# Kernel optimization log

Hardware: AMD Instinct MI355X
Metric: run time of the kernel (lower is better)

The kernel has to match this reference:

```python
import jax, jax.numpy as jnp
import numpy as np

B, L, D = 4, 4096, 1024
DS, EXP, DC = 16, 2, 4
DI = EXP * D
K_SYM = max(3, 2 * DC + 1)  # 9


def _linear(x, w, b):
    # torch nn.Linear: y = x @ W^T + b, W:[out,in]
    return jnp.einsum('blc,oc->blo', x, w) + b


def _dwconv(x, kernel, bias, pad_l, pad_r):
    # x:[B,L,C], kernel:[C,1,k] depthwise, torch 'same' padding (asymmetric for even k)
    y = jax.lax.conv_general_dilated(
        x.transpose(0, 2, 1), kernel, window_strides=(1,),
        padding=[(pad_l, pad_r)], dimension_numbers=('NCH', 'OIH', 'NCH'),
        feature_group_count=x.shape[-1])
    return y.transpose(0, 2, 1) + bias


def _rmsnorm(x, w, eps=1e-6):
    scale = jax.lax.rsqrt(jnp.mean(x * x, axis=-1, keepdims=True) + eps)
    return w * x * scale


def setup_inputs() -> dict:
    key = jax.random.key(0)
    ks = jax.random.split(key, 12)
    def n(k, shape, s=0.02):
        return jax.random.normal(k, shape, jnp.float32) * s
    return {
        'x': jax.random.normal(ks[0], (B, L, D), jnp.float32),
        'norm_w': jnp.ones((D,), jnp.float32),
        'in_w': n(ks[1], (2 * DI, D)), 'in_b': jnp.zeros((2 * DI,), jnp.float32),
        'dwa_k': n(ks[2], (DI, 1, DC)), 'dwa_b': jnp.zeros((DI,), jnp.float32),
        'A': n(ks[3], (DI, DS)), 'Bm': n(ks[4], (DS, DI)),
        'sym_k': n(ks[5], (DI, 1, K_SYM)), 'sym_b': jnp.zeros((DI,), jnp.float32),
        'pw_w': n(ks[6], (DI, DI)), 'pw_b': jnp.zeros((DI,), jnp.float32),
        'ha_w': n(ks[7], (DI // 2, DI)), 'ha_b': jnp.zeros((DI // 2,), jnp.float32),
        'hb_w': n(ks[8], (DI // 2, DI)), 'hb_b': jnp.zeros((DI // 2,), jnp.float32),
        'fuse_w': n(ks[9], (DI, DI)), 'fuse_b': jnp.zeros((DI,), jnp.float32),
        'out_w': n(ks[10], (D, DI)), 'out_b': jnp.zeros((D,), jnp.float32),
    }


def reference(x, norm_w, in_w, in_b, dwa_k, dwa_b, A, Bm, sym_k, sym_b,
              pw_w, pw_b, ha_w, ha_b, hb_w, hb_b, fuse_w, fuse_b, out_w, out_b):
    residual = x
    h = _rmsnorm(x, norm_w)
    h = _linear(h, in_w, in_b)                       # [B,L,2*DI]
    gate, val = h[..., :DI], h[..., DI:]
    gate = jax.nn.sigmoid(gate)
    # mamba-like branch: depthwise conv (k=4, torch 'same' -> pad (1,2)) + low-rank A@B
    a = _dwconv(val, dwa_k, dwa_b, 1, 2)             # [B,L,DI]
    a = jnp.einsum('bld,ds->bls', a, A)              # [B,L,DS]
    a = jnp.einsum('bls,sd->bld', a, Bm)             # [B,L,DI]
    # symmetric conv branch: depthwise conv (k=9, pad (4,4)) -> silu -> pointwise linear
    b = _dwconv(val, sym_k, sym_b, K_SYM // 2, K_SYM // 2)
    b = jax.nn.silu(b)
    b = _linear(b, pw_w, pw_b)
    a = _linear(a, ha_w, ha_b)                       # [B,L,DI/2]
    b = _linear(b, hb_w, hb_b)                       # [B,L,DI/2]
    y = jnp.concatenate([a, b], axis=-1)             # [B,L,DI]
    y = _linear(y, fuse_w, fuse_b)
    y = gate * y
    y = _linear(y, out_w, out_b)                     # [B,L,D]
    return residual + y
```

## Files before the change

kernel.cpp:

```cpp
#include <hip/hip_runtime.h>
#include <hip/hip_bf16.h>
#include <stdint.h>

typedef __bf16 bf16;
typedef __bf16 bf16x8 __attribute__((ext_vector_type(8)));
typedef __bf16 bf16x4 __attribute__((ext_vector_type(4)));
typedef float  f32x4  __attribute__((ext_vector_type(4)));

#define LDS_PTR(p) ((__attribute__((address_space(3))) uint32_t*)(p))
#define GLB_PTR(p) ((const __attribute__((address_space(1))) uint32_t*)(p))

static constexpr int BATCH = 4, SEQ = 4096, DMODEL = 1024;
static constexpr int DI = 2048;
static constexpr int MTOK = BATCH * SEQ;

enum { EPI_SPLIT = 0, EPI_PLAIN = 1, EPI_GATEADD = 2, EPI_RES = 3, EPI_F32S = 4 };

template <int EPI, bool SPLITK = false>
__global__ __launch_bounds__(256) void gemm_bt(
    const bf16* __restrict__ Aact, const bf16* __restrict__ W,
    const float* __restrict__ bias,
    bf16* __restrict__ out0, bf16* __restrict__ out1,
    const bf16* __restrict__ gate,
    float* __restrict__ outf, const float* __restrict__ resid,
    int N, int K, int ldC, int col_off)
{
  __shared__ __align__(16) bf16 sA[128 * 64];
  __shared__ __align__(16) bf16 sB[128 * 64];
  const int tid  = threadIdx.x;
  int n0, m0, kbeg, kend;
  size_t out_off = 0;
  if (SPLITK) {
    n0 = blockIdx.z * 128;
    m0 = blockIdx.y * 128;
    const int kh = K / gridDim.x;
    kbeg = blockIdx.x * kh; kend = kbeg + kh;
    out_off = (EPI == EPI_F32S) ? (size_t)blockIdx.x * (size_t)col_off
                                : (size_t)blockIdx.x * ((size_t)MTOK * 128);
  } else {
    const int nT  = gridDim.x;
    const int lin = blockIdx.y * nT + blockIdx.x;
    const int grp = lin / (8 * nT);
    const int within = lin - grp * (8 * nT);
    n0 = (within >> 3) * 128;
    m0 = (grp * 8 + (within & 7)) * 128;
    kbeg = 0; kend = K;
  }
  const int lane = tid & 63;
  const int wv   = tid >> 6;
  const int wr   = wv >> 1, wc = wv & 1;
  const int l15  = lane & 15, quad = lane >> 4;

  f32x4 acc[4][4];
#pragma unroll
  for (int i = 0; i < 4; ++i)
#pragma unroll
    for (int j = 0; j < 4; ++j) acc[i][j] = (f32x4){0.f, 0.f, 0.f, 0.f};

  int rr[4], cb[4];
#pragma unroll
  for (int j = 0; j < 4; ++j) {
    const int s = tid + j * 256;
    rr[j] = s >> 3;
    cb[j] = ((s & 7) ^ (rr[j] & 7)) * 16;
  }

  const char* gA = (const char*)(Aact + (size_t)m0 * K);
  const char* gW = (const char*)(W + (size_t)n0 * K);

  for (int k0 = kbeg; k0 < kend; k0 += 64) {
    if (k0 != kbeg) __syncthreads();
#pragma unroll
    for (int j = 0; j < 4; ++j)
      __builtin_amdgcn_global_load_lds(GLB_PTR(gA + ((size_t)rr[j] * K + k0) * 2 + cb[j]),
                                       LDS_PTR(sA + (tid + j * 256) * 8), 16, 0, 0);
#pragma unroll
    for (int j = 0; j < 4; ++j)
      __builtin_amdgcn_global_load_lds(GLB_PTR(gW + ((size_t)rr[j] * K + k0) * 2 + cb[j]),
                                       LDS_PTR(sB + (tid + j * 256) * 8), 16, 0, 0);
    __syncthreads();

#pragma unroll
    for (int h = 0; h < 2; ++h) {
      bf16x8 av[4], bv[4];
#pragma unroll
      for (int t = 0; t < 4; ++t) {
        const int Ra = wr * 64 + t * 16 + l15;
        const int Rb = wc * 64 + t * 16 + l15;
        const int cc = h * 4 + quad;
        av[t] = *(const bf16x8*)(sA + (Ra * 8 + (cc ^ (Ra & 7))) * 8);
        bv[t] = *(const bf16x8*)(sB + (Rb * 8 + (cc ^ (Rb & 7))) * 8);
      }
#pragma unroll
      for (int i = 0; i < 4; ++i)
#pragma unroll
        for (int j = 0; j < 4; ++j)
          acc[i][j] = __builtin_amdgcn_mfma_f32_16x16x32_bf16(av[i], bv[j], acc[i][j], 0, 0, 0);
    }
  }

  bf16*  o0 = out0 + out_off;
  float* of = outf ? outf + out_off : nullptr;
#pragma unroll
  for (int i = 0; i < 4; ++i) {
    const int mbase = m0 + wr * 64 + i * 16 + quad * 4;
#pragma unroll
    for (int j = 0; j < 4; ++j) {
      const int n = n0 + wc * 64 + j * 16 + l15;
      const float bj = bias ? bias[n] : 0.f;
#pragma unroll
      for (int r = 0; r < 4; ++r) {
        const int mm = mbase + r;
        float v = acc[i][j][r] + bj;
        if (EPI == EPI_SPLIT) {
          if (n < DI) o0[(size_t)mm * DI + n] = (bf16)(1.f / (1.f + __expf(-v)));
          else        out1[(size_t)mm * DI + (n - DI)] = (bf16)v;
        } else if (EPI == EPI_PLAIN) {
          o0[(size_t)mm * ldC + col_off + n] = (bf16)v;
        } else if (EPI == EPI_GATEADD) {
          const size_t idx = (size_t)mm * ldC + n;
          float zz = (float)o0[idx];
          float g  = (float)gate[(size_t)mm * DI + n];
          o0[idx] = (bf16)((v + zz) * g);
        } else if (EPI == EPI_F32S) {
          of[(size_t)mm * ldC + n] = v;
        } else {
          outf[(size_t)mm * ldC + n] = v + resid[(size_t)mm * ldC + n];
        }
      }
    }
  }
}

__global__ __launch_bounds__(256) void rmsnorm_kernel(
    const float* __restrict__ x, const float* __restrict__ w, bf16* __restrict__ out)
{
  const int row = blockIdx.x;
  const int tid = threadIdx.x;
  const float4 xv = ((const float4*)(x + (size_t)row * DMODEL))[tid];
  float s = xv.x * xv.x + xv.y * xv.y + xv.z * xv.z + xv.w * xv.w;
#pragma unroll
  for (int o = 32; o; o >>= 1) s += __shfl_xor(s, o);
  __shared__ float red[4];
  if ((tid & 63) == 0) red[tid >> 6] = s;
  __syncthreads();
  const float tot = red[0] + red[1] + red[2] + red[3];
  const float scale = rsqrtf(tot * (1.f / DMODEL) + 1e-6f);
  const float4 wv = ((const float4*)w)[tid];
  bf16x4 o4 = { (bf16)(xv.x * wv.x * scale), (bf16)(xv.y * wv.y * scale),
                (bf16)(xv.z * wv.z * scale), (bf16)(xv.w * wv.w * scale) };
  *(bf16x4*)(out + (size_t)row * DMODEL + tid * 4) = o4;
}

static constexpr int TL2 = 32;
__global__ __launch_bounds__(256) void conv_kernel(
    const bf16* __restrict__ val,
    const float* __restrict__ sym_k, const float* __restrict__ sym_b,
    bf16* __restrict__ bbuf)
{
  const int d  = (blockIdx.y * 256 + threadIdx.x) * 4;
  const int b  = blockIdx.z;
  const int l0 = blockIdx.x * TL2;
  float wk[9][4], bs[4];
#pragma unroll
  for (int j = 0; j < 4; ++j) {
    bs[j] = sym_b[d + j];
#pragma unroll
    for (int k = 0; k < 9; ++k) wk[k][j] = sym_k[(d + j) * 9 + k];
  }
  const bf16* base = val + (size_t)b * SEQ * DI + d;

  float win[9][4];
#pragma unroll
  for (int j = 0; j < 8; ++j) {
    const int xr = l0 + j - 4;
    if (xr >= 0 && xr < SEQ) {
      bf16x4 v = *(const bf16x4*)(base + (size_t)xr * DI);
#pragma unroll
      for (int c = 0; c < 4; ++c) win[j][c] = (float)v[c];
    } else {
#pragma unroll
      for (int c = 0; c < 4; ++c) win[j][c] = 0.f;
    }
  }
  for (int t = 0; t < TL2; ++t) {
    const int xf = l0 + t + 4;
    if (xf < SEQ) {
      bf16x4 v = *(const bf16x4*)(base + (size_t)xf * DI);
#pragma unroll
      for (int c = 0; c < 4; ++c) win[8][c] = (float)v[c];
    } else {
#pragma unroll
      for (int c = 0; c < 4; ++c) win[8][c] = 0.f;
    }
    float sb[4];
#pragma unroll
    for (int c = 0; c < 4; ++c) sb[c] = bs[c];
#pragma unroll
    for (int k = 0; k < 9; ++k)
#pragma unroll
      for (int c = 0; c < 4; ++c) sb[c] += win[k][c] * wk[k][c];
    bf16x4 o;
#pragma unroll
    for (int c = 0; c < 4; ++c) o[c] = (bf16)(sb[c] / (1.f + __expf(-sb[c])));
    *(bf16x4*)(bbuf + ((size_t)b * SEQ + l0 + t) * DI + d) = o;
#pragma unroll
    for (int k = 0; k < 8; ++k)
#pragma unroll
      for (int c = 0; c < 4; ++c) win[k][c] = win[k + 1][c];
  }
}

__global__ __launch_bounds__(256) void prep_cvt_kernel(
    const float* __restrict__ in_w, const float* __restrict__ hb_w,
    const float* __restrict__ out_w,
    bf16* __restrict__ in_wbf, bf16* __restrict__ hb_bf, bf16* __restrict__ out_bf)
{
  const int b = blockIdx.x;
  const float* src; bf16* dst; size_t i;
  if (b < 4096)      { src = in_w;  dst = in_wbf; i = (size_t)b * 256 + threadIdx.x; }
  else if (b < 6144) { src = hb_w;  dst = hb_bf;  i = (size_t)(b - 4096) * 256 + threadIdx.x; }
  else               { src = out_w; dst = out_bf; i = (size_t)(b - 6144) * 256 + threadIdx.x; }
  const float4 v = ((const float4*)src)[i];
  bf16x4 o4 = { (bf16)v.x, (bf16)v.y, (bf16)v.z, (bf16)v.w };
  *(bf16x4*)(dst + 4 * i) = o4;
}

__global__ __launch_bounds__(256) void transpose_kernel(
    const float* __restrict__ in, bf16* __restrict__ out)
{
  __shared__ float s[32][33];
  const int tid = threadIdx.x;
  const int r = tid >> 5, x = tid & 31;
  const int c0 = blockIdx.y * 32, d0 = blockIdx.x * 32;
#pragma unroll
  for (int rr = r; rr < 32; rr += 8)
    s[rr][x] = in[(size_t)(c0 + rr) * 2048 + d0 + x];
  __syncthreads();
#pragma unroll
  for (int rr = r; rr < 32; rr += 8)
    out[(size_t)(d0 + rr) * 2048 + c0 + x] = (bf16)s[x][rr];
}

__global__ __launch_bounds__(256) void prep_small_kernel(
    const float* __restrict__ Bm, const float* __restrict__ ha_w,
    const float* __restrict__ dwa_b, const float* __restrict__ dwa_k,
    const float* __restrict__ A,
    const float* __restrict__ hb_w, const float* __restrict__ pw_b,
    const float* __restrict__ hb_b, const float* __restrict__ fuse_w,
    const float* __restrict__ Hp,
    float* __restrict__ T1, float* __restrict__ cvec, float* __restrict__ b_H,
    bf16* __restrict__ Wp, bf16* __restrict__ Fb, bf16* __restrict__ Ht)
{
  const int b = blockIdx.x, tid = threadIdx.x;
  __shared__ float red[4][16];
  if (b < 1024) {
    const int o = b;
    float acc[16];
#pragma unroll
    for (int s = 0; s < 16; ++s) acc[s] = 0.f;
    for (int d = tid; d < 2048; d += 256) {
      const float w = ha_w[(size_t)o * 2048 + d];
#pragma unroll
      for (int s = 0; s < 16; ++s) acc[s] += Bm[s * 2048 + d] * w;
    }
    const int lane = tid & 63, wv = tid >> 6;
#pragma unroll
    for (int s = 0; s < 16; ++s) {
      float v = acc[s];
#pragma unroll
      for (int off = 32; off; off >>= 1) v += __shfl_xor(v, off);
      if (lane == s) red[wv][s] = v;
    }
    __syncthreads();
    if (tid < 16)
      T1[tid * 1024 + o] = red[0][tid] + red[1][tid] + red[2][tid] + red[3][tid];
  } else if (b == 1024) {
    float acc[16];
#pragma unroll
    for (int s = 0; s < 16; ++s) acc[s] = 0.f;
    for (int d = tid; d < 2048; d += 256) {
      const float w = dwa_b[d];
#pragma unroll
      for (int s = 0; s < 16; ++s) acc[s] += w * A[d * 16 + s];
    }
    const int lane = tid & 63, wv = tid >> 6;
#pragma unroll
    for (int s = 0; s < 16; ++s) {
      float v = acc[s];
#pragma unroll
      for (int off = 32; off; off >>= 1) v += __shfl_xor(v, off);
      if (lane == s) red[wv][s] = v;
    }
    __syncthreads();
    if (tid < 16) cvec[tid] = red[0][tid] + red[1][tid] + red[2][tid] + red[3][tid];
  } else if (b < 1029) {
    const int o = (b - 1025) * 256 + tid;
    float acc = hb_b[o];
    const float* hr = hb_w + (size_t)o * 2048;
    for (int c = 0; c < 2048; c += 4) {
      float4 h = *(const float4*)(hr + c);
      float4 p = *(const float4*)(pw_b + c);
      acc += h.x * p.x + h.y * p.y + h.z * p.z + h.w * p.w;
    }
    b_H[o] = acc;
  } else if (b < 1037) {
    const int d = (b - 1029) * 256 + tid;
    float kk[4], av[16];
#pragma unroll
    for (int k = 0; k < 4; ++k) kk[k] = dwa_k[d * 4 + k];
#pragma unroll
    for (int s = 0; s < 16; ++s) av[s] = A[d * 16 + s];
#pragma unroll
    for (int k = 0; k < 4; ++k)
#pragma unroll
      for (int s = 0; s < 16; ++s)
        Wp[(size_t)(k * 16 + s) * 2048 + d] = (bf16)(kk[k] * av[s]);
    for (int n = 64; n < 128; ++n) Wp[(size_t)n * 2048 + d] = (bf16)0.f;
  } else if (b < 3085) {
    const int idx = (b - 1037) * 256 + tid;
    const int n = idx >> 8, o4 = idx & 255;
    float4 v = ((const float4*)(fuse_w + (size_t)n * 2048 + 1024))[o4];
    bf16x4 o = { (bf16)v.x, (bf16)v.y, (bf16)v.z, (bf16)v.w };
    *(bf16x4*)(Fb + (size_t)n * 1024 + o4 * 4) = o;
  } else {
    const size_t e4 = (size_t)(b - 3085) * 256 + tid;
    float4 p0 = ((const float4*)Hp)[e4];
    float4 p1 = ((const float4*)(Hp + 2048 * 1024))[e4];
    bf16x4 o = { (bf16)(p0.x + p1.x), (bf16)(p0.y + p1.y),
                 (bf16)(p0.z + p1.z), (bf16)(p0.w + p1.w) };
    *(bf16x4*)(Ht + e4 * 4) = o;
  }
}

__global__ __launch_bounds__(256) void prep_fuse_kernel(
    const float* __restrict__ T1, const float* __restrict__ fuse_w,
    const float* __restrict__ fuse_b, const float* __restrict__ ha_b,
    const float* __restrict__ b_H,
    float* __restrict__ T2t, float* __restrict__ bias_z)
{
  const int b = blockIdx.x, tid = threadIdx.x;
  if (b < 128) {
    const int n = b * 16 + (tid >> 4);
    const int s = tid & 15;
    const float* fr = fuse_w + (size_t)n * 2048;
    const float* tr = T1 + s * 1024;
    float acc = 0.f;
    for (int o = 0; o < 1024; o += 4) {
      float4 f = *(const float4*)(fr + o);
      float4 t = *(const float4*)(tr + o);
      acc += f.x * t.x + f.y * t.y + f.z * t.z + f.w * t.w;
    }
    T2t[n * 16 + s] = acc;
  } else {
    const int n = b - 128;
    const float* fr = fuse_w + (size_t)n * 2048;
    const int o = tid * 4;
    float4 fa = *(const float4*)(fr + o);
    float4 fb = *(const float4*)(fr + 1024 + o);
    float4 ha = *(const float4*)(ha_b + o);
    float4 bh = *(const float4*)(b_H + o);
    float acc = fa.x * ha.x + fa.y * ha.y + fa.z * ha.z + fa.w * ha.w
              + fb.x * bh.x + fb.y * bh.y + fb.z * bh.z + fb.w * bh.w;
#pragma unroll
    for (int off = 32; off; off >>= 1) acc += __shfl_xor(acc, off);
    __shared__ float r4[4];
    if ((tid & 63) == 0) r4[tid >> 6] = acc;
    __syncthreads();
    if (tid == 0) bias_z[n] = fuse_b[n] + r4[0] + r4[1] + r4[2] + r4[3];
  }
}

__global__ __launch_bounds__(256) void za_kernel(
    const bf16* __restrict__ P0, const bf16* __restrict__ P1,
    const float* __restrict__ T2t,
    const float* __restrict__ cvec, const float* __restrict__ bias_z,
    bf16* __restrict__ z)
{
  __shared__ float s16t[32][16];
  const int tid = threadIdx.x;
  const int tok0 = blockIdx.x * 32;
  for (int p = tid; p < 512; p += 256) {
    const int t = p >> 4, s = p & 15;
    const int tok = tok0 + t;
    const int l = tok & (SEQ - 1), bb = tok >> 12;
    float acc = cvec[s];
#pragma unroll
    for (int k = 0; k < 4; ++k) {
      const int r = l - 1 + k;
      if ((unsigned)r < (unsigned)SEQ) {
        const size_t idx = ((size_t)bb * SEQ + r) * 128 + k * 16 + s;
        acc += (float)P0[idx] + (float)P1[idx];
      }
    }
    s16t[t][s] = acc;
  }
  const int c0 = tid * 8;
  float t2[8][16], bz[8];
#pragma unroll
  for (int j = 0; j < 8; ++j) {
    bz[j] = bias_z[c0 + j];
#pragma unroll
    for (int q = 0; q < 4; ++q) {
      float4 v = ((const float4*)(T2t + (size_t)(c0 + j) * 16))[q];
      t2[j][q * 4 + 0] = v.x; t2[j][q * 4 + 1] = v.y;
      t2[j][q * 4 + 2] = v.z; t2[j][q * 4 + 3] = v.w;
    }
  }
  __syncthreads();
  for (int t = 0; t < 32; ++t) {
    float sv[16];
#pragma unroll
    for (int s = 0; s < 16; ++s) sv[s] = s16t[t][s];
    bf16x8 o;
#pragma unroll
    for (int j = 0; j < 8; ++j) {
      float a = bz[j];
#pragma unroll
      for (int s = 0; s < 16; ++s) a += sv[s] * t2[j][s];
      o[j] = (bf16)a;
    }
    *(bf16x8*)(z + (size_t)(tok0 + t) * 2048 + c0) = o;
  }
}

extern "C" void kernel_launch(void* const* d_in, const int* in_sizes, int n_in,
                              void* d_out, int out_size, void* d_ws, size_t ws_size,
                              hipStream_t stream)
{
  const float* x      = (const float*)d_in[0];
  const float* norm_w = (const float*)d_in[1];
  const float* in_w   = (const float*)d_in[2];
  const float* in_b   = (const float*)d_in[3];
  const float* dwa_k  = (const float*)d_in[4];
  const float* dwa_b  = (const float*)d_in[5];
  const float* Amat   = (const float*)d_in[6];
  const float* Bm     = (const float*)d_in[7];
  const float* sym_k  = (const float*)d_in[8];
  const float* sym_b  = (const float*)d_in[9];
  const float* pw_w   = (const float*)d_in[10];
  const float* pw_b   = (const float*)d_in[11];
  const float* ha_w   = (const float*)d_in[12];
  const float* ha_b   = (const float*)d_in[13];
  const float* hb_w   = (const float*)d_in[14];
  const float* hb_b   = (const float*)d_in[15];
  const float* fuse_w = (const float*)d_in[16];
  const float* fuse_b = (const float*)d_in[17];
  const float* out_w  = (const float*)d_in[18];
  const float* out_b  = (const float*)d_in[19];
  float* out = (float*)d_out;

  char* ws = (char*)d_ws;
  const size_t MB = 1u << 20, KB = 1u << 10;
  bf16*  in_wbf  = (bf16*)(ws + 0);
  bf16*  hnorm   = (bf16*)(ws + 8 * MB);
  bf16*  bsilu   = (bf16*)(ws + 0);
  float* Hpart   = (float*)(ws + 64 * MB);
  bf16*  valp    = (bf16*)(ws + 64 * MB);
  bf16*  zbuf    = (bf16*)(ws + 64 * MB);
  bf16*  gatep   = (bf16*)(ws + 128 * MB);
  bf16*  Pbuf    = (bf16*)(ws + 192 * MB);
  bf16*  pwT_bf  = (bf16*)(ws + 200 * MB);
  bf16*  WB_bf   = (bf16*)(ws + 200 * MB);
  bf16*  hb_bf   = (bf16*)(ws + 208 * MB);
  bf16*  Fb_bf   = (bf16*)(ws + 208 * MB);
  bf16*  Ht_bf   = (bf16*)(ws + 212 * MB);
  bf16*  out_bf  = (bf16*)(ws + 216 * MB);
  float* T1      = (float*)(ws + 220 * MB);
  float* cvec    = (float*)(ws + 220 * MB + 64 * KB);
  float* b_H     = (float*)(ws + 220 * MB + 68 * KB);
  float* bias_z  = (float*)(ws + 220 * MB + 72 * KB);
  bf16*  Wp      = (bf16*)(ws + 220 * MB + 80 * KB);
  float* T2t     = (float*)(ws + 220 * MB + 592 * KB);

  prep_cvt_kernel<<<8192, 256, 0, stream>>>(in_w, hb_w, out_w, in_wbf, hb_bf, out_bf);
  transpose_kernel<<<dim3(64, 64), 256, 0, stream>>>(pw_w, pwT_bf);
  gemm_bt<EPI_F32S, true><<<dim3(2, 16, 8), 256, 0, stream>>>(
      pwT_bf, hb_bf, nullptr, nullptr, nullptr, nullptr, Hpart, nullptr,
      1024, 2048, 1024, 2048 * 1024);
  prep_small_kernel<<<5133, 256, 0, stream>>>(
      Bm, ha_w, dwa_b, dwa_k, Amat, hb_w, pw_b, hb_b, fuse_w, Hpart,
      T1, cvec, b_H, Wp, Fb_bf, Ht_bf);
  gemm_bt<EPI_PLAIN><<<dim3(16, 16), 256, 0, stream>>>(
      Fb_bf, Ht_bf, nullptr, WB_bf, nullptr, nullptr, nullptr, nullptr, 2048, 1024, 2048, 0);
  prep_fuse_kernel<<<2176, 256, 0, stream>>>(T1, fuse_w, fuse_b, ha_b, b_H, T2t, bias_z);

  rmsnorm_kernel<<<MTOK, 256, 0, stream>>>(x, norm_w, hnorm);
  gemm_bt<EPI_SPLIT><<<dim3(32, 128), 256, 0, stream>>>(
      hnorm, in_wbf, in_b, gatep, valp, nullptr, nullptr, nullptr, 4096, 1024, DI, 0);
  conv_kernel<<<dim3(SEQ / TL2, 2, BATCH), 256, 0, stream>>>(
      valp, sym_k, sym_b, bsilu);
  gemm_bt<EPI_PLAIN, true><<<dim3(2, 128), 256, 0, stream>>>(
      valp, Wp, nullptr, Pbuf, nullptr, nullptr, nullptr, nullptr, 128, 2048, 128, 0);
  za_kernel<<<MTOK / 32, 256, 0, stream>>>(
      Pbuf, Pbuf + (size_t)MTOK * 128, T2t, cvec, bias_z, zbuf);
  gemm_bt<EPI_GATEADD><<<dim3(16, 128), 256, 0, stream>>>(
      bsilu, WB_bf, nullptr, zbuf, nullptr, gatep, nullptr, nullptr, 2048, 2048, 2048, 0);
  gemm_bt<EPI_RES><<<dim3(8, 128), 256, 0, stream>>>(
      zbuf, out_bf, out_b, nullptr, nullptr, nullptr, out, x, 1024, 2048, 1024, 0);
}
```

Measured before the change: 882.7 us.

## Fuse rank-16 z contribution into gated GEMM epilogue and merge prep kernels

The old za_kernel wrote a full 16K x 2048 bf16 z buffer, and the gated GEMM then read it back in its epilogue. Now a small kernel computes only the per-token 16-vector s16, and the GEMM epilogue computes the rank-16 product with T2 in registers, staged through LDS. This removes a large intermediate write and read. The pw_w transpose is also merged into the weight-conversion launch to save one kernel launch. The cost is extra epilogue FLOPs, higher register pressure (tt[4][16] plus sv[16]) and an added LDS sync in the GEMM.

```diff
diff --git a/kernel.cpp b/kernel.cpp
--- a/kernel.cpp
+++ b/kernel.cpp
@@ -14,7 +14,7 @@
 static constexpr int DI = 2048;
 static constexpr int MTOK = BATCH * SEQ;
 
-enum { EPI_SPLIT = 0, EPI_PLAIN = 1, EPI_GATEADD = 2, EPI_RES = 3, EPI_F32S = 4 };
+enum { EPI_SPLIT = 0, EPI_PLAIN = 1, EPI_ZGATE = 2, EPI_RES = 3, EPI_F32S = 4 };
 
 template <int EPI, bool SPLITK = false>
 __global__ __launch_bounds__(256) void gemm_bt(
@@ -99,29 +99,66 @@
     }
   }
 
+  float* sS = (float*)sA;
+  float* sT = (float*)sB;
+  float tt[4][16];
+  if (EPI == EPI_ZGATE) {
+    __syncthreads();
+    const float* s16f = outf;
+    const float* T2   = resid;
+    {
+      const float4 a0 = ((const float4*)(s16f + (size_t)m0 * 16))[tid * 2];
+      const float4 a1 = ((const float4*)(s16f + (size_t)m0 * 16))[tid * 2 + 1];
+      const float4 b0 = ((const float4*)(T2 + (size_t)n0 * 16))[tid * 2];
+      const float4 b1 = ((const float4*)(T2 + (size_t)n0 * 16))[tid * 2 + 1];
+      const int i0 = tid * 8;
+      const float av_[8] = {a0.x, a0.y, a0.z, a0.w, a1.x, a1.y, a1.z, a1.w};
+      const float bv_[8] = {b0.x, b0.y, b0.z, b0.w, b1.x, b1.y, b1.z, b1.w};
+#pragma unroll
+      for (int e = 0; e < 8; ++e) {
+        const int idx = i0 + e;
+        sS[(idx >> 4) * 17 + (idx & 15)] = av_[e];
+        sT[(idx >> 4) * 17 + (idx & 15)] = bv_[e];
+      }
+    }
+    __syncthreads();
+#pragma unroll
+    for (int j = 0; j < 4; ++j) {
+      const int nloc = wc * 64 + j * 16 + l15;
+#pragma unroll
+      for (int s = 0; s < 16; ++s) tt[j][s] = sT[nloc * 17 + s];
+    }
+  }
+
   bf16*  o0 = out0 + out_off;
   float* of = outf ? outf + out_off : nullptr;
 #pragma unroll
   for (int i = 0; i < 4; ++i) {
     const int mbase = m0 + wr * 64 + i * 16 + quad * 4;
 #pragma unroll
-    for (int j = 0; j < 4; ++j) {
-      const int n = n0 + wc * 64 + j * 16 + l15;
-      const float bj = bias ? bias[n] : 0.f;
-#pragma unroll
-      for (int r = 0; r < 4; ++r) {
-        const int mm = mbase + r;
+    for (int r = 0; r < 4; ++r) {
+      const int mm = mbase + r;
+      float sv[16];
+      if (EPI == EPI_ZGATE) {
+        const int mloc = wr * 64 + i * 16 + quad * 4 + r;
+#pragma unroll
+        for (int s = 0; s < 16; ++s) sv[s] = sS[mloc * 17 + s];
+      }
+#pragma unroll
+      for (int j = 0; j < 4; ++j) {
+        const int n = n0 + wc * 64 + j * 16 + l15;
+        const float bj = bias ? bias[n] : 0.f;
         float v = acc[i][j][r] + bj;
         if (EPI == EPI_SPLIT) {
           if (n < DI) o0[(size_t)mm * DI + n] = (bf16)(1.f / (1.f + __expf(-v)));
           else        out1[(size_t)mm * DI + (n - DI)] = (bf16)v;
         } else if (EPI == EPI_PLAIN) {
           o0[(size_t)mm * ldC + col_off + n] = (bf16)v;
-        } else if (EPI == EPI_GATEADD) {
-          const size_t idx = (size_t)mm * ldC + n;
-          float zz = (float)o0[idx];
-          float g  = (float)gate[(size_t)mm * DI + n];
-          o0[idx] = (bf16)((v + zz) * g);
+        } else if (EPI == EPI_ZGATE) {
+#pragma unroll
+          for (int s = 0; s < 16; ++s) v += sv[s] * tt[j][s];
+          const float g = (float)gate[(size_t)mm * DI + n];
+          o0[(size_t)mm * ldC + n] = (bf16)(v * g);
         } else if (EPI == EPI_F32S) {
           of[(size_t)mm * ldC + n] = v;
         } else {
@@ -213,33 +250,33 @@
 
 __global__ __launch_bounds__(256) void prep_cvt_kernel(
     const float* __restrict__ in_w, const float* __restrict__ hb_w,
-    const float* __restrict__ out_w,
-    bf16* __restrict__ in_wbf, bf16* __restrict__ hb_bf, bf16* __restrict__ out_bf)
-{
+    const float* __restrict__ out_w, const float* __restrict__ pw_w,
+    bf16* __restrict__ in_wbf, bf16* __restrict__ hb_bf,
+    bf16* __restrict__ out_bf, bf16* __restrict__ pwT_bf)
+{
+  __shared__ float s[32][33];
   const int b = blockIdx.x;
-  const float* src; bf16* dst; size_t i;
-  if (b < 4096)      { src = in_w;  dst = in_wbf; i = (size_t)b * 256 + threadIdx.x; }
-  else if (b < 6144) { src = hb_w;  dst = hb_bf;  i = (size_t)(b - 4096) * 256 + threadIdx.x; }
-  else               { src = out_w; dst = out_bf; i = (size_t)(b - 6144) * 256 + threadIdx.x; }
-  const float4 v = ((const float4*)src)[i];
-  bf16x4 o4 = { (bf16)v.x, (bf16)v.y, (bf16)v.z, (bf16)v.w };
-  *(bf16x4*)(dst + 4 * i) = o4;
-}
-
-__global__ __launch_bounds__(256) void transpose_kernel(
-    const float* __restrict__ in, bf16* __restrict__ out)
-{
-  __shared__ float s[32][33];
   const int tid = threadIdx.x;
-  const int r = tid >> 5, x = tid & 31;
-  const int c0 = blockIdx.y * 32, d0 = blockIdx.x * 32;
-#pragma unroll
-  for (int rr = r; rr < 32; rr += 8)
-    s[rr][x] = in[(size_t)(c0 + rr) * 2048 + d0 + x];
-  __syncthreads();
-#pragma unroll
-  for (int rr = r; rr < 32; rr += 8)
-    out[(size_t)(d0 + rr) * 2048 + c0 + x] = (bf16)s[x][rr];
+  if (b < 8192) {
+    const float* src; bf16* dst; size_t i;
+    if (b < 4096)      { src = in_w;  dst = in_wbf; i = (size_t)b * 256 + tid; }
+    else if (b < 6144) { src = hb_w;  dst = hb_bf;  i = (size_t)(b - 4096) * 256 + tid; }
+    else               { src = out_w; dst = out_bf; i = (size_t)(b - 6144) * 256 + tid; }
+    const float4 v = ((const float4*)src)[i];
+    bf16x4 o4 = { (bf16)v.x, (bf16)v.y, (bf16)v.z, (bf16)v.w };
+    *(bf16x4*)(dst + 4 * i) = o4;
+  } else {
+    const int q = b - 8192;
+    const int d0 = (q & 63) * 32, c0 = (q >> 6) * 32;
+    const int r = tid >> 5, x = tid & 31;
+#pragma unroll
+    for (int rr = r; rr < 32; rr += 8)
+      s[rr][x] = pw_w[(size_t)(c0 + rr) * 2048 + d0 + x];
+    __syncthreads();
+#pragma unroll
+    for (int rr = r; rr < 32; rr += 8)
+      pwT_bf[(size_t)(d0 + rr) * 2048 + c0 + x] = (bf16)s[x][rr];
+  }
 }
 
 __global__ __launch_bounds__(256) void prep_small_kernel(
@@ -371,57 +408,23 @@
   }
 }
 
-__global__ __launch_bounds__(256) void za_kernel(
+__global__ __launch_bounds__(256) void s16_kernel(
     const bf16* __restrict__ P0, const bf16* __restrict__ P1,
-    const float* __restrict__ T2t,
-    const float* __restrict__ cvec, const float* __restrict__ bias_z,
-    bf16* __restrict__ z)
-{
-  __shared__ float s16t[32][16];
-  const int tid = threadIdx.x;
-  const int tok0 = blockIdx.x * 32;
-  for (int p = tid; p < 512; p += 256) {
-    const int t = p >> 4, s = p & 15;
-    const int tok = tok0 + t;
-    const int l = tok & (SEQ - 1), bb = tok >> 12;
-    float acc = cvec[s];
-#pragma unroll
-    for (int k = 0; k < 4; ++k) {
-      const int r = l - 1 + k;
-      if ((unsigned)r < (unsigned)SEQ) {
-        const size_t idx = ((size_t)bb * SEQ + r) * 128 + k * 16 + s;
-        acc += (float)P0[idx] + (float)P1[idx];
-      }
-    }
-    s16t[t][s] = acc;
-  }
-  const int c0 = tid * 8;
-  float t2[8][16], bz[8];
-#pragma unroll
-  for (int j = 0; j < 8; ++j) {
-    bz[j] = bias_z[c0 + j];
-#pragma unroll
-    for (int q = 0; q < 4; ++q) {
-      float4 v = ((const float4*)(T2t + (size_t)(c0 + j) * 16))[q];
-      t2[j][q * 4 + 0] = v.x; t2[j][q * 4 + 1] = v.y;
-      t2[j][q * 4 + 2] = v.z; t2[j][q * 4 + 3] = v.w;
-    }
-  }
-  __syncthreads();
-  for (int t = 0; t < 32; ++t) {
-    float sv[16];
-#pragma unroll
-    for (int s = 0; s < 16; ++s) sv[s] = s16t[t][s];
-    bf16x8 o;
-#pragma unroll
-    for (int j = 0; j < 8; ++j) {
-      float a = bz[j];
-#pragma unroll
-      for (int s = 0; s < 16; ++s) a += sv[s] * t2[j][s];
-      o[j] = (bf16)a;
-    }
-    *(bf16x8*)(z + (size_t)(tok0 + t) * 2048 + c0) = o;
-  }
+    const float* __restrict__ cvec, float* __restrict__ s16f)
+{
+  const int g = blockIdx.x * 256 + threadIdx.x;
+  const int tok = g >> 4, s = g & 15;
+  const int l = tok & (SEQ - 1), bb = tok >> 12;
+  float acc = cvec[s];
+#pragma unroll
+  for (int k = 0; k < 4; ++k) {
+    const int r = l - 1 + k;
+    if ((unsigned)r < (unsigned)SEQ) {
+      const size_t idx = ((size_t)bb * SEQ + r) * 128 + k * 16 + s;
+      acc += (float)P0[idx] + (float)P1[idx];
+    }
+  }
+  s16f[(size_t)tok * 16 + s] = acc;
 }
 
 extern "C" void kernel_launch(void* const* d_in, const int* in_sizes, int n_in,
@@ -464,6 +467,7 @@
   bf16*  WB_bf   = (bf16*)(ws + 200 * MB);
   bf16*  hb_bf   = (bf16*)(ws + 208 * MB);
   bf16*  Fb_bf   = (bf16*)(ws + 208 * MB);
+  float* s16f    = (float*)(ws + 208 * MB);
   bf16*  Ht_bf   = (bf16*)(ws + 212 * MB);
   bf16*  out_bf  = (bf16*)(ws + 216 * MB);
   float* T1      = (float*)(ws + 220 * MB);
@@ -473,8 +477,8 @@
   bf16*  Wp      = (bf16*)(ws + 220 * MB + 80 * KB);
   float* T2t     = (float*)(ws + 220 * MB + 592 * KB);
 
-  prep_cvt_kernel<<<8192, 256, 0, stream>>>(in_w, hb_w, out_w, in_wbf, hb_bf, out_bf);
-  transpose_kernel<<<dim3(64, 64), 256, 0, stream>>>(pw_w, pwT_bf);
+  prep_cvt_kernel<<<12288, 256, 0, stream>>>(
+      in_w, hb_w, out_w, pw_w, in_wbf, hb_bf, out_bf, pwT_bf);
   gemm_bt<EPI_F32S, true><<<dim3(2, 16, 8), 256, 0, stream>>>(
       pwT_bf, hb_bf, nullptr, nullptr, nullptr, nullptr, Hpart, nullptr,
       1024, 2048, 1024, 2048 * 1024);
@@ -492,10 +496,10 @@
       valp, sym_k, sym_b, bsilu);
   gemm_bt<EPI_PLAIN, true><<<dim3(2, 128), 256, 0, stream>>>(
       valp, Wp, nullptr, Pbuf, nullptr, nullptr, nullptr, nullptr, 128, 2048, 128, 0);
-  za_kernel<<<MTOK / 32, 256, 0, stream>>>(
-      Pbuf, Pbuf + (size_t)MTOK * 128, T2t, cvec, bias_z, zbuf);
-  gemm_bt<EPI_GATEADD><<<dim3(16, 128), 256, 0, stream>>>(
-      bsilu, WB_bf, nullptr, zbuf, nullptr, gatep, nullptr, nullptr, 2048, 2048, 2048, 0);
+  s16_kernel<<<MTOK * 16 / 256, 256, 0, stream>>>(
+      Pbuf, Pbuf + (size_t)MTOK * 128, cvec, s16f);
+  gemm_bt<EPI_ZGATE><<<dim3(16, 128), 256, 0, stream>>>(
+      bsilu, WB_bf, bias_z, zbuf, nullptr, gatep, s16f, T2t, 2048, 2048, 2048, 0);
   gemm_bt<EPI_RES><<<dim3(8, 128), 256, 0, stream>>>(
       zbuf, out_bf, out_b, nullptr, nullptr, nullptr, out, x, 1024, 2048, 1024, 0);
 }
```

Measured after the change: 949.8 us. 7.6% more time.
